# Performance work log

Measured on AMD Instinct MI355X. Metric: run time of the kernel, lower is better.

The kernel has to match this reference:

```python
import jax, jax.numpy as jnp
import numpy as np

B, L, CIN = 32768, 35, 21
N_FLANK, C_FLANK, PEP_MAX = 10, 10, 15
F, K, H = 128, 9, 64


def setup_inputs() -> dict:
    key = jax.random.key(0)
    ks = jax.random.split(key, 16)
    s = lambda k, shape, scale=0.05: jax.random.normal(k, shape, dtype=jnp.float32) * scale
    return {
        "sequence": jax.random.normal(ks[0], (B, L, CIN), dtype=jnp.float32),
        "peptide_length": jax.random.randint(ks[1], (B,), 5, PEP_MAX + 1, dtype=jnp.int32),
        # main conv, weight in WIO layout (k, in, out)
        "conv_w": s(ks[2], (K, CIN, F)),
        "conv_b": jnp.zeros((F,), jnp.float32),
        # n-flank post 1x1 convs (as matmuls)
        "n_w1": s(ks[3], (F, H)), "n_b1": jnp.zeros((H,), jnp.float32),
        "n_w2": s(ks[4], (H, 1)), "n_b2": jnp.zeros((1,), jnp.float32),
        # c-flank post 1x1 convs
        "c_w1": s(ks[5], (F, H)), "c_b1": jnp.zeros((H,), jnp.float32),
        "c_w2": s(ks[6], (H, 1)), "c_b2": jnp.zeros((1,), jnp.float32),
        # flank-average dense layers
        "navg_w": s(ks[7], (F, 1)), "navg_b": jnp.zeros((1,), jnp.float32),
        "cavg_w": s(ks[8], (F, 1)), "cavg_b": jnp.zeros((1,), jnp.float32),
        # output layer: init ones / zeros as in the torch module
        "out_w": jnp.ones((6, 1), jnp.float32),
        "out_b": jnp.zeros((1,), jnp.float32),
    }


def _post(x, w1, b1, w2, b2):
    # stack of 1x1 convs: relu on hidden, tanh on final single-output layer
    h = jax.nn.relu(jnp.einsum("blf,fh->blh", x, w1) + b1)
    return jnp.tanh(jnp.einsum("blh,ho->blo", h, w2) + b2)  # [B, L, 1]


def _masked_neg_max(y, mask):
    # torch: max over dim1 of (y+1)*mask, minus 1, negated
    m = mask[..., None].astype(y.dtype)
    return -(jnp.max((y + 1.0) * m, axis=1) - 1.0)  # [B, 1]


def reference(sequence, peptide_length, conv_w, conv_b, n_w1, n_b1, n_w2, n_b2,
              c_w1, c_b1, c_w2, c_b2, navg_w, navg_b, cavg_w, cavg_b, out_w, out_b):
    # main conv, padding='same', relu activation (dropout rate 0 -> no-op)
    x = jax.lax.conv_general_dilated(
        sequence, conv_w, window_strides=(1,), padding="SAME",
        dimension_numbers=("NWC", "WIO", "NWC"))
    conv_result = jax.nn.relu(x + conv_b)  # [B, L, F]

    plen = peptide_length.reshape(-1)
    pos = jnp.arange(L)[None, :]  # [1, L]

    # --- n-flank branch ---
    yn = _post(conv_result, n_w1, n_b1, n_w2, n_b2)  # [B, L, 1]
    cleaved_n = yn[:, N_FLANK, :]  # [B, 1]
    mask_n = (pos >= N_FLANK + 1) & (pos < (N_FLANK + plen)[:, None])
    maxpool_n = _masked_neg_max(yn, mask_n)
    avg_n = jnp.tanh(jnp.mean(conv_result[:, :N_FLANK], axis=1) @ navg_w + navg_b)

    # --- c-flank branch ---
    yc = _post(conv_result, c_w1, c_b1, c_w2, c_b2)  # [B, L, 1]
    c_idx = (N_FLANK + plen - 1).astype(jnp.int32)
    cleaved_c = jnp.take_along_axis(yc, c_idx[:, None, None], axis=1)[:, 0, :]  # [B, 1]
    mask_c = (pos >= N_FLANK) & (pos < (N_FLANK + plen - 1)[:, None])
    maxpool_c = _masked_neg_max(yc, mask_c)
    starts = (N_FLANK + plen)[:, None]
    mask_cf = ((pos >= starts) & (pos < starts + C_FLANK))[..., None].astype(conv_result.dtype)
    s = jnp.sum((conv_result + 1.0) * mask_cf, axis=1)  # [B, F]
    cnt = jnp.clip(jnp.sum(mask_cf, axis=1), 1.0, None)
    avg_c = jnp.tanh((s / cnt - 1.0) @ cavg_w + cavg_b)

    combined = jnp.concatenate(
        [cleaved_n, maxpool_n, avg_n, cleaved_c, maxpool_c, avg_c], axis=-1)  # [B, 6]
    out = jax.nn.sigmoid(combined @ out_w + out_b)
    return out[:, 0]  # [B]
```

## Files before the change

### kernel.cpp

```cpp
#include <hip/hip_runtime.h>
#include <hip/hip_bf16.h>
#include <math.h>

#define Ln     35
#define CINn   21
#define CINP   24
#define Fn     128
#define Kn     9
#define Hn     64
#define GB     16
#define SEQ_STRIDE 1064
#define TILE_STRIDE 136
#define YP_STRIDE 136
#define NYL    16

typedef __attribute__((ext_vector_type(8))) short short8;
typedef __attribute__((ext_vector_type(4))) float f32x4;

static __device__ __forceinline__ unsigned short bf16bits(float f) {
    __hip_bfloat16 h = __float2bfloat16(f);
    return *(unsigned short*)&h;
}

template <int CTRL>
static __device__ __forceinline__ float dpp_add(float v) {
    int r = __builtin_amdgcn_update_dpp(0, __builtin_bit_cast(int, v),
                                        CTRL, 0xF, 0xF, true);
    return v + __builtin_bit_cast(float, r);
}
static __device__ __forceinline__ float row_sum16(float v) {
    v = dpp_add<0x128>(v);
    v = dpp_add<0x124>(v);
    v = dpp_add<0x122>(v);
    v = dpp_add<0x121>(v);
    return v;
}

__global__ __launch_bounds__(512, 4) void fused_kernel(
    const float* __restrict__ seq,    const int*   __restrict__ plen_arr,
    const float* __restrict__ conv_w, const float* __restrict__ conv_b,
    const float* __restrict__ n_w1,   const float* __restrict__ n_b1,
    const float* __restrict__ n_w2,   const float* __restrict__ n_b2,
    const float* __restrict__ c_w1,   const float* __restrict__ c_b1,
    const float* __restrict__ c_w2,   const float* __restrict__ c_b2,
    const float* __restrict__ navg_w, const float* __restrict__ navg_b,
    const float* __restrict__ cavg_w, const float* __restrict__ cavg_b,
    const float* __restrict__ out_w,  const float* __restrict__ out_b,
    float* __restrict__ out)
{
    __shared__ __align__(16) unsigned short s_seq[GB * SEQ_STRIDE];
    __shared__ __align__(16) unsigned short s_tile[2][GB * TILE_STRIDE];
    __shared__ __align__(16) float s_yp[NYL * YP_STRIDE];
    float* s_y   = (float*)s_seq;
    float* s_avg = (float*)s_seq + 1152;

    const int t    = threadIdx.x;
    const int wave = t >> 6;
    const int lane = t & 63;
    const int quad = lane >> 4;
    const int col  = lane & 15;
    const int b0   = blockIdx.x * GB;

    {
        uint4* p = (uint4*)s_seq;
        for (int i = t; i < (GB * SEQ_STRIDE) / 8; i += 512)
            p[i] = make_uint4(0u, 0u, 0u, 0u);
    }

    short8 wb[7];
    short8 w1b[4];
    float  cbias[4], b1v, w2v;
    const int head = wave >> 2;
    {
        const int ng = wave * 16 + col;
        #pragma unroll
        for (int s = 0; s < 7; s++) {
            short8 v;
            #pragma unroll
            for (int j = 0; j < 8; j++) {
                int kk = 32 * s + quad * 8 + j;
                int k = kk / CINP, c = kk % CINP;
                float f = (k < Kn && c < CINn) ? conv_w[(k * CINn + c) * Fn + ng] : 0.0f;
                v[j] = (short)bf16bits(f);
            }
            wb[s] = v;
        }
        const int nl = ng & 63;
        #pragma unroll
        for (int s = 0; s < 4; s++) {
            short8 v;
            #pragma unroll
            for (int j = 0; j < 8; j++) {
                int k = 32 * s + quad * 8 + j;
                float f = head ? c_w1[k * Hn + nl] : n_w1[k * Hn + nl];
                v[j] = (short)bf16bits(f);
            }
            w1b[s] = v;
        }
        #pragma unroll
        for (int r = 0; r < 4; r++)
            cbias[r] = conv_b[wave * 16 + 4 * quad + r];
        b1v = head ? c_b1[nl] : n_b1[nl];
        w2v = head ? c_w2[nl] : n_w2[nl];
    }
    const int plen_lane = plen_arr[b0 + col];

    __syncthreads();

    {
        const float4* gsrc = (const float4*)(seq + (size_t)b0 * (Ln * CINn));
        for (int i = t; i < (GB * Ln * CINn) / 4; i += 512) {
            int i4 = i * 4;
            int bi = i4 / (Ln * CINn), r = i4 - bi * (Ln * CINn);
            int l = r / CINn, c = r - l * CINn;
            float4 v = gsrc[i];
            int base = bi * SEQ_STRIDE + (4 + l) * CINP + c;
            #pragma unroll
            for (int j = 0; j < 4; j++) {
                float fj = (j == 0) ? v.x : (j == 1) ? v.y : (j == 2) ? v.z : v.w;
                int adj = ((c + j >= CINn) ? 3 : 0) + ((r + j >= Ln * CINn) ? 224 : 0);
                s_seq[base + j + adj] = bf16bits(fj);
            }
        }
    }
    __syncthreads();

    float sum_n[4] = {0.f,0.f,0.f,0.f};
    float sum_c[4] = {0.f,0.f,0.f,0.f};

    for (int l0 = 0; l0 < 36; l0 += 2) {
        const int l1 = l0 + 1;
        short8 af0[7], af1[7];
        #pragma unroll
        for (int s = 0; s < 7; s++) {
            af0[s] = *(const short8*)&s_seq[col * SEQ_STRIDE + l0 * CINP + 32 * s + quad * 8];
            af1[s] = *(const short8*)&s_seq[col * SEQ_STRIDE + l1 * CINP + 32 * s + quad * 8];
        }
        f32x4 cacc0 = {0.f,0.f,0.f,0.f};
        f32x4 cacc1 = {0.f,0.f,0.f,0.f};
        #pragma unroll
        for (int s = 0; s < 7; s++) {
            cacc0 = __builtin_amdgcn_mfma_f32_16x16x32_bf16(wb[s], af0[s], cacc0, 0, 0, 0);
            cacc1 = __builtin_amdgcn_mfma_f32_16x16x32_bf16(wb[s], af1[s], cacc1, 0, 0, 0);
        }
        float a0 = fmaxf(cacc0[0] + cbias[0], 0.0f);
        float a1 = fmaxf(cacc0[1] + cbias[1], 0.0f);
        float a2 = fmaxf(cacc0[2] + cbias[2], 0.0f);
        float a3 = fmaxf(cacc0[3] + cbias[3], 0.0f);
        float e0 = fmaxf(cacc1[0] + cbias[0], 0.0f);
        float e1 = fmaxf(cacc1[1] + cbias[1], 0.0f);
        float e2 = fmaxf(cacc1[2] + cbias[2], 0.0f);
        float e3 = fmaxf(cacc1[3] + cbias[3], 0.0f);
        {
            float cm0 = (l0 >= 10 + plen_lane && l0 < 20 + plen_lane) ? 1.0f : 0.0f;
            float cm1 = (l1 >= 10 + plen_lane && l1 < 20 + plen_lane) ? 1.0f : 0.0f;
            if (l0 < 10) {
                sum_n[0] += a0; sum_n[1] += a1; sum_n[2] += a2; sum_n[3] += a3;
            }
            if (l1 < 10) {
                sum_n[0] += e0; sum_n[1] += e1; sum_n[2] += e2; sum_n[3] += e3;
            }
            sum_c[0] += cm0 * a0 + cm1 * e0;
            sum_c[1] += cm0 * a1 + cm1 * e1;
            sum_c[2] += cm0 * a2 + cm1 * e2;
            sum_c[3] += cm0 * a3 + cm1 * e3;
        }

        if (l0 >= 10 && l0 < 26) {
            ushort4 pk0 = { bf16bits(a0), bf16bits(a1), bf16bits(a2), bf16bits(a3) };
            ushort4 pk1 = { bf16bits(e0), bf16bits(e1), bf16bits(e2), bf16bits(e3) };
            *(ushort4*)&s_tile[0][col * TILE_STRIDE + wave * 16 + 4 * quad] = pk0;
            *(ushort4*)&s_tile[1][col * TILE_STRIDE + wave * 16 + 4 * quad] = pk1;
            __syncthreads();

            short8 am0[4], am1[4];
            #pragma unroll
            for (int s = 0; s < 4; s++) {
                am0[s] = *(const short8*)&s_tile[0][col * TILE_STRIDE + 32 * s + quad * 8];
                am1[s] = *(const short8*)&s_tile[1][col * TILE_STRIDE + 32 * s + quad * 8];
            }
            f32x4 hacc0 = {0.f,0.f,0.f,0.f};
            f32x4 hacc1 = {0.f,0.f,0.f,0.f};
            #pragma unroll
            for (int s = 0; s < 4; s++) {
                hacc0 = __builtin_amdgcn_mfma_f32_16x16x32_bf16(am0[s], w1b[s], hacc0, 0, 0, 0);
                hacc1 = __builtin_amdgcn_mfma_f32_16x16x32_bf16(am1[s], w1b[s], hacc1, 0, 0, 0);
            }
            float p0[4], p1[4];
            #pragma unroll
            for (int r = 0; r < 4; r++) {
                p0[r] = row_sum16(fmaxf(hacc0[r] + b1v, 0.f) * w2v);
                p1[r] = row_sum16(fmaxf(hacc1[r] + b1v, 0.f) * w2v);
            }
            if (col == 0) {
                *(f32x4*)&s_yp[(l0 - 10) * YP_STRIDE + wave * 16 + quad * 4] =
                    (f32x4){p0[0], p0[1], p0[2], p0[3]};
                *(f32x4*)&s_yp[(l1 - 10) * YP_STRIDE + wave * 16 + quad * 4] =
                    (f32x4){p1[0], p1[1], p1[2], p1[3]};
            }
            __syncthreads();
        }
    }
    __syncthreads();

    {
        float an = 0.f, ac = 0.f;
        #pragma unroll
        for (int r = 0; r < 4; r++) {
            int fidx = wave * 16 + 4 * quad + r;
            an += sum_n[r] * navg_w[fidx];
            ac += sum_c[r] * cavg_w[fidx];
        }
        an += __shfl_xor(an, 16); an += __shfl_xor(an, 32);
        ac += __shfl_xor(ac, 16); ac += __shfl_xor(ac, 32);
        if (quad == 0) {
            s_avg[wave * 2 * GB + 0 * GB + col] = an;
            s_avg[wave * 2 * GB + 1 * GB + col] = ac;
        }
    }
    __syncthreads();

    {
        const float bn = n_b2[0], bc = c_b2[0];
        for (int i = t; i < 2 * GB * NYL; i += 512) {
            int m = i & 15, rem = i >> 4;
            int li = rem & 15, hd = rem >> 4;
            float v = (hd ? bc : bn);
            #pragma unroll
            for (int w = 0; w < 4; w++)
                v += s_yp[li * YP_STRIDE + (hd * 4 + w) * 16 + m];
            s_y[hd * GB * 36 + m * 36 + (10 + li)] = tanhf(v);
        }
    }
    __syncthreads();

    if (t < GB) {
        const int m = t;
        const int plen = plen_arr[b0 + m];
        const float* ym = s_y + m * 36;
        const float* yc = s_y + GB * 36 + m * 36;
        float cleaved_n = ym[10];
        float mn = 0.f;
        for (int l = 11; l < 10 + plen; l++) mn = fmaxf(mn, ym[l] + 1.f);
        float maxpool_n = -(mn - 1.f);
        float cleaved_c = yc[10 + plen - 1];
        float mc = 0.f;
        for (int l = 10; l < 10 + plen - 1; l++) mc = fmaxf(mc, yc[l] + 1.f);
        float maxpool_c = -(mc - 1.f);
        float sn = 0.f, sc = 0.f;
        #pragma unroll
        for (int w = 0; w < 8; w++) {
            sn += s_avg[w * 2 * GB + 0 * GB + m];
            sc += s_avg[w * 2 * GB + 1 * GB + m];
        }
        float avg_n = tanhf(sn * 0.1f + navg_b[0]);
        float avg_c = tanhf(sc * 0.1f + cavg_b[0]);
        float comb = cleaved_n * out_w[0] + maxpool_n * out_w[1] + avg_n * out_w[2]
                   + cleaved_c * out_w[3] + maxpool_c * out_w[4] + avg_c * out_w[5]
                   + out_b[0];
        out[b0 + m] = 1.f / (1.f + expf(-comb));
    }
}

extern "C" void kernel_launch(void* const* d_in, const int* in_sizes, int n_in,
                              void* d_out, int out_size, void* d_ws, size_t ws_size,
                              hipStream_t stream) {
    const int B = in_sizes[1];
    fused_kernel<<<B / GB, 512, 0, stream>>>(
        (const float*)d_in[0],  (const int*)d_in[1],
        (const float*)d_in[2],  (const float*)d_in[3],
        (const float*)d_in[4],  (const float*)d_in[5],
        (const float*)d_in[6],  (const float*)d_in[7],
        (const float*)d_in[8],  (const float*)d_in[9],
        (const float*)d_in[10], (const float*)d_in[11],
        (const float*)d_in[12], (const float*)d_in[13],
        (const float*)d_in[14], (const float*)d_in[15],
        (const float*)d_in[16], (const float*)d_in[17],
        (float*)d_out);
}
```

Before: 308.8 us.

## Quad-buffer hidden tile, remap post-MLP work per wave, drop per-iteration barrier

```diff
diff --git a/kernel.cpp b/kernel.cpp
--- a/kernel.cpp
+++ b/kernel.cpp
@@ -49,7 +49,7 @@
     float* __restrict__ out)
 {
     __shared__ __align__(16) unsigned short s_seq[GB * SEQ_STRIDE];
-    __shared__ __align__(16) unsigned short s_tile[2][GB * TILE_STRIDE];
+    __shared__ __align__(16) unsigned short s_tile[4][GB * TILE_STRIDE];
     __shared__ __align__(16) float s_yp[NYL * YP_STRIDE];
     float* s_y   = (float*)s_seq;
     float* s_avg = (float*)s_seq + 1152;
@@ -60,6 +60,8 @@
     const int quad = lane >> 4;
     const int col  = lane & 15;
     const int b0   = blockIdx.x * GB;
+    const int lsel = wave >> 2;
+    const int t0   = 2 * (wave & 3);
 
     {
         uint4* p = (uint4*)s_seq;
@@ -68,9 +70,8 @@
     }
 
     short8 wb[7];
-    short8 w1b[4];
-    float  cbias[4], b1v, w2v;
-    const int head = wave >> 2;
+    short8 w1b[2][4];
+    float  cbias[4], b1v[2], w2v[2];
     {
         const int ng = wave * 16 + col;
         #pragma unroll
@@ -85,23 +86,28 @@
             }
             wb[s] = v;
         }
-        const int nl = ng & 63;
-        #pragma unroll
-        for (int s = 0; s < 4; s++) {
-            short8 v;
-            #pragma unroll
-            for (int j = 0; j < 8; j++) {
-                int k = 32 * s + quad * 8 + j;
-                float f = head ? c_w1[k * Hn + nl] : n_w1[k * Hn + nl];
-                v[j] = (short)bf16bits(f);
-            }
-            w1b[s] = v;
+        #pragma unroll
+        for (int j = 0; j < 2; j++) {
+            const int nt = t0 + j;
+            const int nl = (nt * 16 + col) & 63;
+            const int hj = nt >= 4;
+            #pragma unroll
+            for (int s = 0; s < 4; s++) {
+                short8 v;
+                #pragma unroll
+                for (int jj = 0; jj < 8; jj++) {
+                    int k = 32 * s + quad * 8 + jj;
+                    float f = hj ? c_w1[k * Hn + nl] : n_w1[k * Hn + nl];
+                    v[jj] = (short)bf16bits(f);
+                }
+                w1b[j][s] = v;
+            }
+            b1v[j] = hj ? c_b1[nl] : n_b1[nl];
+            w2v[j] = hj ? c_w2[nl] : n_w2[nl];
         }
         #pragma unroll
         for (int r = 0; r < 4; r++)
             cbias[r] = conv_b[wave * 16 + 4 * quad + r];
-        b1v = head ? c_b1[nl] : n_b1[nl];
-        w2v = head ? c_w2[nl] : n_w2[nl];
     }
     const int plen_lane = plen_arr[b0 + col];
 
@@ -130,19 +136,28 @@
 
     for (int l0 = 0; l0 < 36; l0 += 2) {
         const int l1 = l0 + 1;
-        short8 af0[7], af1[7];
-        #pragma unroll
-        for (int s = 0; s < 7; s++) {
-            af0[s] = *(const short8*)&s_seq[col * SEQ_STRIDE + l0 * CINP + 32 * s + quad * 8];
-            af1[s] = *(const short8*)&s_seq[col * SEQ_STRIDE + l1 * CINP + 32 * s + quad * 8];
-        }
         f32x4 cacc0 = {0.f,0.f,0.f,0.f};
+        {
+            short8 af[7];
+            #pragma unroll
+            for (int s = 0; s < 7; s++)
+                af[s] = *(const short8*)&s_seq[col * SEQ_STRIDE + l0 * CINP + 32 * s + quad * 8];
+            #pragma unroll
+            for (int s = 0; s < 7; s++)
+                cacc0 = __builtin_amdgcn_mfma_f32_16x16x32_bf16(wb[s], af[s], cacc0, 0, 0, 0);
+        }
+        __builtin_amdgcn_sched_barrier(0);
         f32x4 cacc1 = {0.f,0.f,0.f,0.f};
-        #pragma unroll
-        for (int s = 0; s < 7; s++) {
-            cacc0 = __builtin_amdgcn_mfma_f32_16x16x32_bf16(wb[s], af0[s], cacc0, 0, 0, 0);
-            cacc1 = __builtin_amdgcn_mfma_f32_16x16x32_bf16(wb[s], af1[s], cacc1, 0, 0, 0);
-        }
+        {
+            short8 af[7];
+            #pragma unroll
+            for (int s = 0; s < 7; s++)
+                af[s] = *(const short8*)&s_seq[col * SEQ_STRIDE + l1 * CINP + 32 * s + quad * 8];
+            #pragma unroll
+            for (int s = 0; s < 7; s++)
+                cacc1 = __builtin_amdgcn_mfma_f32_16x16x32_bf16(wb[s], af[s], cacc1, 0, 0, 0);
+        }
+        __builtin_amdgcn_sched_barrier(0);
         float a0 = fmaxf(cacc0[0] + cbias[0], 0.0f);
         float a1 = fmaxf(cacc0[1] + cbias[1], 0.0f);
         float a2 = fmaxf(cacc0[2] + cbias[2], 0.0f);
@@ -169,37 +184,37 @@
         if (l0 >= 10 && l0 < 26) {
             ushort4 pk0 = { bf16bits(a0), bf16bits(a1), bf16bits(a2), bf16bits(a3) };
             ushort4 pk1 = { bf16bits(e0), bf16bits(e1), bf16bits(e2), bf16bits(e3) };
-            *(ushort4*)&s_tile[0][col * TILE_STRIDE + wave * 16 + 4 * quad] = pk0;
-            *(ushort4*)&s_tile[1][col * TILE_STRIDE + wave * 16 + 4 * quad] = pk1;
+            *(ushort4*)&s_tile[l0 & 3][col * TILE_STRIDE + wave * 16 + 4 * quad] = pk0;
+            *(ushort4*)&s_tile[l1 & 3][col * TILE_STRIDE + wave * 16 + 4 * quad] = pk1;
             __syncthreads();
 
-            short8 am0[4], am1[4];
+            const int myl = l0 + lsel;
+            short8 am[4];
+            #pragma unroll
+            for (int s = 0; s < 4; s++)
+                am[s] = *(const short8*)&s_tile[myl & 3][col * TILE_STRIDE + 32 * s + quad * 8];
+            f32x4 h0 = {0.f,0.f,0.f,0.f};
+            f32x4 h1 = {0.f,0.f,0.f,0.f};
             #pragma unroll
             for (int s = 0; s < 4; s++) {
-                am0[s] = *(const short8*)&s_tile[0][col * TILE_STRIDE + 32 * s + quad * 8];
-                am1[s] = *(const short8*)&s_tile[1][col * TILE_STRIDE + 32 * s + quad * 8];
-            }
-            f32x4 hacc0 = {0.f,0.f,0.f,0.f};
-            f32x4 hacc1 = {0.f,0.f,0.f,0.f};
-            #pragma unroll
-            for (int s = 0; s < 4; s++) {
-                hacc0 = __builtin_amdgcn_mfma_f32_16x16x32_bf16(am0[s], w1b[s], hacc0, 0, 0, 0);
-                hacc1 = __builtin_amdgcn_mfma_f32_16x16x32_bf16(am1[s], w1b[s], hacc1, 0, 0, 0);
+                h0 = __builtin_amdgcn_mfma_f32_16x16x32_bf16(am[s], w1b[0][s], h0, 0, 0, 0);
+                h1 = __builtin_amdgcn_mfma_f32_16x16x32_bf16(am[s], w1b[1][s], h1, 0, 0, 0);
             }
             float p0[4], p1[4];
             #pragma unroll
             for (int r = 0; r < 4; r++) {
-                p0[r] = row_sum16(fmaxf(hacc0[r] + b1v, 0.f) * w2v);
-                p1[r] = row_sum16(fmaxf(hacc1[r] + b1v, 0.f) * w2v);
+                p0[r] = row_sum16(fmaxf(h0[r] + b1v[0], 0.f) * w2v[0]);
+                p1[r] = row_sum16(fmaxf(h1[r] + b1v[1], 0.f) * w2v[1]);
             }
             if (col == 0) {
-                *(f32x4*)&s_yp[(l0 - 10) * YP_STRIDE + wave * 16 + quad * 4] =
+                const int rowb = (myl - 10) * YP_STRIDE;
+                *(f32x4*)&s_yp[rowb + t0 * 16 + quad * 4] =
                     (f32x4){p0[0], p0[1], p0[2], p0[3]};
-                *(f32x4*)&s_yp[(l1 - 10) * YP_STRIDE + wave * 16 + quad * 4] =
+                *(f32x4*)&s_yp[rowb + (t0 + 1) * 16 + quad * 4] =
                     (f32x4){p1[0], p1[1], p1[2], p1[3]};
             }
-            __syncthreads();
-        }
+        }
+        __builtin_amdgcn_sched_barrier(0);
     }
     __syncthreads();
 
```

After: 349.1 us. 1.13x slower.
